# Performance work log

Hardware: AMD Instinct MI355X
Metric: run time of the kernel (lower is better)

## Reference

```python
import jax, jax.numpy as jnp
import numpy as np


def exp_mix_frac(p1, p2, a1, b1, a2, b2):
    # stable merge of two (numerator, denominator) pairs carried in log-scale p
    p = jnp.maximum(p1, p2)
    e1 = jnp.exp(p1 - p)
    e2 = jnp.exp(p2 - p)
    return a1 * e1 + a2 * e2, b1 * e1 + b2 * e2, p


def assoc_reduce_step(left, right):
    akv_l, ak_l, w_l, p_l = left
    akv_r, ak_r, w_r, p_r = right
    a, b, p = exp_mix_frac(p_l + w_r, p_r, akv_l, ak_l, akv_r, ak_r)
    return a, b, w_l + w_r, p


def setup_inputs() -> dict:
    key = jax.random.key(0)
    ks = jax.random.split(key, 7)
    S, B, E = 2048, 8, 1024
    scale = 1.0 / np.sqrt(E)
    return {
        "x": jax.random.normal(ks[0], (S, B, E), jnp.float32),
        "tmrkv": jax.random.uniform(ks[1], (3 * E,), jnp.float32),
        "Wk": jax.random.normal(ks[2], (E, E), jnp.float32) * scale,
        "Wv": jax.random.normal(ks[3], (E, E), jnp.float32) * scale,
        "time_decay": jax.random.normal(ks[4], (E,), jnp.float32) - 1.0,
        "time_first": jax.random.normal(ks[5], (E,), jnp.float32),
        "Wout": jax.random.normal(ks[6], (E, E), jnp.float32) * scale,
    }


def reference(x, tmrkv, Wk, Wv, time_decay, time_first, Wout):
    # x: (S, B, E) time-major (batch_first=False path of the source module)
    S, B, E = x.shape
    x_prev = jnp.concatenate([jnp.zeros_like(x[:1]), x[:-1]], axis=0)
    # time_mix_rkv layout: [r | k | v]; r-branch is computed in the source but
    # never used in the associative-scan path, so it is omitted (same output).
    mk = tmrkv[E:2 * E]
    mv = tmrkv[2 * E:]
    k = (mk * x + (1.0 - mk) * x_prev) @ Wk  # (S, B, E)
    v = (mv * x + (1.0 - mv) * x_prev) @ Wv  # (S, B, E)

    k_ = k.reshape(S, B * E)
    v_ = v.reshape(S, B * E)
    W_ = jnp.broadcast_to(jnp.tile(time_decay, B)[None, :], (S, B * E))
    ones = jnp.ones_like(v_)
    # log-depth parallel scan over time with numerically-stable exp merge
    a_, b_, _, p_ = jax.lax.associative_scan(
        assoc_reduce_step, (v_, ones, W_, k_), axis=0)

    a_state = a_.reshape(S, B, E)
    b_state = b_.reshape(S, B, E)
    p_state = p_.reshape(S, B, E)
    c, d, _ = exp_mix_frac(p_state, k + time_first + time_decay,
                           a_state, b_state, v, jnp.ones_like(v))
    rwkv = c / d  # (S, B, E)
    return rwkv @ Wout
```

## Files before the change

### kernel.cpp

```cpp
#include <hip/hip_runtime.h>
#include <stdint.h>

#define S_LEN  2048
#define B_DIM  8
#define E_DIM  1024
#define BE     (B_DIM * E_DIM)
#define M_ROWS (S_LEN * B_DIM)
#define NCHUNK 64
#define CLEN   (S_LEN / NCHUNK)

typedef __attribute__((ext_vector_type(8))) short bf16x8;
typedef __attribute__((ext_vector_type(4))) float f32x4;

__device__ __forceinline__ unsigned short f2bf(float f) {
    unsigned int u = __float_as_uint(f);
    u += 0x7FFFu + ((u >> 16) & 1u);
    return (unsigned short)(u >> 16);
}

__global__ __launch_bounds__(256) void mix_kernel(
    const float* __restrict__ x, const float* __restrict__ tmrkv,
    unsigned short* __restrict__ xk, unsigned short* __restrict__ xv)
{
    int i = blockIdx.x * 256 + threadIdx.x;
    const float4* x4 = (const float4*)x;
    float4 xc = x4[i];
    float4 xp = make_float4(0.f, 0.f, 0.f, 0.f);
    if (i >= BE / 4) xp = x4[i - BE / 4];
    int e4 = i & (E_DIM / 4 - 1);
    float4 mk = ((const float4*)(tmrkv + E_DIM))[e4];
    float4 mv = ((const float4*)(tmrkv + 2 * E_DIM))[e4];
    ushort4 ok, ov;
    ok.x = f2bf(mk.x * xc.x + (1.f - mk.x) * xp.x);
    ok.y = f2bf(mk.y * xc.y + (1.f - mk.y) * xp.y);
    ok.z = f2bf(mk.z * xc.z + (1.f - mk.z) * xp.z);
    ok.w = f2bf(mk.w * xc.w + (1.f - mk.w) * xp.w);
    ov.x = f2bf(mv.x * xc.x + (1.f - mv.x) * xp.x);
    ov.y = f2bf(mv.y * xc.y + (1.f - mv.y) * xp.y);
    ov.z = f2bf(mv.z * xc.z + (1.f - mv.z) * xp.z);
    ov.w = f2bf(mv.w * xc.w + (1.f - mv.w) * xp.w);
    ((ushort4*)xk)[i] = ok;
    ((ushort4*)xv)[i] = ov;
}

__global__ __launch_bounds__(256) void cast_transpose_k(
    const float* __restrict__ in, unsigned short* __restrict__ out)
{
    __shared__ float tile[32][33];
    int bx = blockIdx.x * 32, by = blockIdx.y * 32;
    int tx = threadIdx.x, ty = threadIdx.y;
    #pragma unroll
    for (int i = 0; i < 32; i += 8)
        tile[ty + i][tx] = in[(size_t)(by + ty + i) * E_DIM + bx + tx];
    __syncthreads();
    #pragma unroll
    for (int i = 0; i < 32; i += 8)
        out[(size_t)(bx + ty + i) * E_DIM + by + tx] = f2bf(tile[tx][ty + i]);
}

#define BM 128
#define BN 128
#define BK 32

__global__ __launch_bounds__(256) void gemm_bf16_bt(
    const unsigned short* __restrict__ A,
    const unsigned short* __restrict__ BT,
    float* __restrict__ C, int M, int N, int K)
{
    __shared__ __align__(16) unsigned short As[BM * BK];
    __shared__ __align__(16) unsigned short Bs[BN * BK];
    const int tid  = threadIdx.x;
    const int wave = tid >> 6, lane = tid & 63;
    const int bm = blockIdx.x * BM, bn = blockIdx.y * BN;
    const int wr = (wave >> 1) * 64, wc = (wave & 1) * 64;
    const int lrow = lane & 15, lq = lane >> 4;

    f32x4 acc[4][4];
    #pragma unroll
    for (int i = 0; i < 4; ++i)
        #pragma unroll
        for (int j = 0; j < 4; ++j)
            acc[i][j] = (f32x4){0.f, 0.f, 0.f, 0.f};

    const int nk = K / BK;
    for (int kt = 0; kt < nk; ++kt) {
        __syncthreads();
        const int kk = kt * BK;
        #pragma unroll
        for (int s = 0; s < 2; ++s) {
            int chunk = s * 256 + wave * 64 + lane;
            int row = chunk >> 2;
            int cb  = (chunk & 3) * 16;
            const char* ga = (const char*)(A  + (size_t)(bm + row) * K + kk) + cb;
            const char* gb = (const char*)(BT + (size_t)(bn + row) * K + kk) + cb;
            char* la = (char*)As + s * 4096 + wave * 1024;
            char* lb = (char*)Bs + s * 4096 + wave * 1024;
            __builtin_amdgcn_global_load_lds(
                (const __attribute__((address_space(1))) unsigned int*)ga,
                (__attribute__((address_space(3))) unsigned int*)la, 16, 0, 0);
            __builtin_amdgcn_global_load_lds(
                (const __attribute__((address_space(1))) unsigned int*)gb,
                (__attribute__((address_space(3))) unsigned int*)lb, 16, 0, 0);
        }
        __syncthreads();

        bf16x8 af[4], bf[4];
        #pragma unroll
        for (int i = 0; i < 4; ++i)
            af[i] = *(const bf16x8*)&As[(wr + i * 16 + lrow) * BK + lq * 8];
        #pragma unroll
        for (int j = 0; j < 4; ++j)
            bf[j] = *(const bf16x8*)&Bs[(wc + j * 16 + lrow) * BK + lq * 8];
        #pragma unroll
        for (int i = 0; i < 4; ++i)
            #pragma unroll
            for (int j = 0; j < 4; ++j)
                acc[i][j] = __builtin_amdgcn_mfma_f32_16x16x32_bf16(
                    af[i], bf[j], acc[i][j], 0, 0, 0);
    }

    #pragma unroll
    for (int i = 0; i < 4; ++i)
        #pragma unroll
        for (int j = 0; j < 4; ++j)
            #pragma unroll
            for (int r = 0; r < 4; ++r) {
                int row = bm + wr + i * 16 + lq * 4 + r;
                int col = bn + wc + j * 16 + lrow;
                C[(size_t)row * N + col] = acc[i][j][r];
            }
}

__global__ __launch_bounds__(256) void scan_pass1(
    const float* __restrict__ k, const float* __restrict__ v,
    const float* __restrict__ tdec,
    float* __restrict__ sA, float* __restrict__ sB, float* __restrict__ sP)
{
    int g  = blockIdx.x * 256 + threadIdx.x;
    int ch = g & (BE - 1);
    int c  = g >> 13;
    float w = tdec[ch & (E_DIM - 1)];
    size_t idx = (size_t)c * CLEN * BE + ch;
    float a = v[idx], bsum = 1.0f, p = k[idx];
    for (int j = 1; j < CLEN; ++j) {
        idx += BE;
        float kt = k[idx], vt = v[idx];
        float pw = p + w;
        float pn = fmaxf(pw, kt);
        float e1 = __expf(pw - pn), e2 = __expf(kt - pn);
        a    = a * e1 + vt * e2;
        bsum = bsum * e1 + e2;
        p    = pn;
    }
    sA[g] = a; sB[g] = bsum; sP[g] = p;
}

__global__ __launch_bounds__(256) void scan_pass2(
    const float* __restrict__ tdec,
    float* __restrict__ sA, float* __restrict__ sB, float* __restrict__ sP)
{
    int ch = blockIdx.x * 256 + threadIdx.x;
    float w  = tdec[ch & (E_DIM - 1)];
    float Lw = (float)CLEN * w;
    float pa = 0.f, pb = 0.f, pp = -__builtin_inff();
    for (int c = 0; c < NCHUNK; ++c) {
        int idx = c * BE + ch;
        float ra = sA[idx], rb = sB[idx], rp = sP[idx];
        sA[idx] = pa; sB[idx] = pb; sP[idx] = pp;
        float pw = pp + Lw;
        float pn = fmaxf(pw, rp);
        float e1 = __expf(pw - pn), e2 = __expf(rp - pn);
        pa = pa * e1 + ra * e2;
        pb = pb * e1 + rb * e2;
        pp = pn;
    }
}

__global__ __launch_bounds__(256) void scan_pass3(
    const float* __restrict__ k, const float* __restrict__ v,
    const float* __restrict__ tdec, const float* __restrict__ tfir,
    const float* __restrict__ sA, const float* __restrict__ sB,
    const float* __restrict__ sP, unsigned short* __restrict__ rwkv)
{
    int g  = blockIdx.x * 256 + threadIdx.x;
    int ch = g & (BE - 1);
    int c  = g >> 13;
    int e  = ch & (E_DIM - 1);
    float w  = tdec[e];
    float u2 = tfir[e] + w;
    float a = sA[g], bsum = sB[g], p = sP[g];
    size_t idx = (size_t)c * CLEN * BE + ch;
    for (int j = 0; j < CLEN; ++j) {
        float kt = k[idx], vt = v[idx];
        float pw = p + w;
        float pn = fmaxf(pw, kt);
        float e1 = __expf(pw - pn), e2 = __expf(kt - pn);
        a    = a * e1 + vt * e2;
        bsum = bsum * e1 + e2;
        p    = pn;
        float kb = kt + u2;
        float q  = fmaxf(p, kb);
        float f1 = __expf(p - q), f2 = __expf(kb - q);
        rwkv[idx] = f2bf((a * f1 + vt * f2) / (bsum * f1 + f2));
        idx += BE;
    }
}

extern "C" void kernel_launch(void* const* d_in, const int* in_sizes, int n_in,
                              void* d_out, int out_size, void* d_ws, size_t ws_size,
                              hipStream_t stream)
{
    const float* x     = (const float*)d_in[0];
    const float* tmrkv = (const float*)d_in[1];
    const float* Wk    = (const float*)d_in[2];
    const float* Wv    = (const float*)d_in[3];
    const float* tdec  = (const float*)d_in[4];
    const float* tfir  = (const float*)d_in[5];
    const float* Wout  = (const float*)d_in[6];
    float* out = (float*)d_out;

    char* ws = (char*)d_ws;
    const size_t SZ_XKV = (size_t)M_ROWS * E_DIM * 2;
    const size_t SZ_KV  = (size_t)M_ROWS * E_DIM * 4;
    unsigned short* xk   = (unsigned short*)(ws);
    unsigned short* xv   = (unsigned short*)(ws + SZ_XKV);
    float* kbuf          = (float*)(ws + 2 * SZ_XKV);
    float* vbuf          = (float*)(ws + 2 * SZ_XKV + SZ_KV);
    unsigned short* WkT  = (unsigned short*)(ws + 2 * SZ_XKV + 2 * SZ_KV);
    unsigned short* WvT  = WkT + (size_t)E_DIM * E_DIM;
    unsigned short* WoutT= WvT + (size_t)E_DIM * E_DIM;
    float* sA = (float*)xv;
    float* sB = sA + (size_t)NCHUNK * BE;
    float* sP = sB + (size_t)NCHUNK * BE;
    unsigned short* rwkv = xk;

    mix_kernel<<<(M_ROWS * E_DIM / 4) / 256, 256, 0, stream>>>(x, tmrkv, xk, xv);

    dim3 tb(32, 8), tg(E_DIM / 32, E_DIM / 32);
    cast_transpose_k<<<tg, tb, 0, stream>>>(Wk,   WkT);
    cast_transpose_k<<<tg, tb, 0, stream>>>(Wv,   WvT);
    cast_transpose_k<<<tg, tb, 0, stream>>>(Wout, WoutT);

    dim3 gg(M_ROWS / BM, E_DIM / BN);
    gemm_bf16_bt<<<gg, 256, 0, stream>>>(xk, WkT, kbuf, M_ROWS, E_DIM, E_DIM);
    gemm_bf16_bt<<<gg, 256, 0, stream>>>(xv, WvT, vbuf, M_ROWS, E_DIM, E_DIM);

    scan_pass1<<<(NCHUNK * BE) / 256, 256, 0, stream>>>(kbuf, vbuf, tdec, sA, sB, sP);
    scan_pass2<<<BE / 256, 256, 0, stream>>>(tdec, sA, sB, sP);
    scan_pass3<<<(NCHUNK * BE) / 256, 256, 0, stream>>>(kbuf, vbuf, tdec, tfir,
                                                        sA, sB, sP, rwkv);

    gemm_bf16_bt<<<gg, 256, 0, stream>>>(rwkv, WoutT, out, M_ROWS, E_DIM, E_DIM);
}
```

Measured before the change: 378.8 us.

## Double GEMM K-tile with XOR-swizzled LDS, parallelize chunk scan, batch weight transposes

Raises the GEMM K-tile from 32 to 64 and XOR-swizzles the 16-byte LDS chunks, so there are half as many barrier-separated iterations and fewer bank conflicts on the fragment reads. The serial 64-step carry scan in scan_pass2 becomes a wave-level log-depth shuffle scan over transposed data in shared memory, launched with four times as many blocks. The three weight cast-transposes are merged into one launch using blockIdx.z. The risks are a larger LDS footprint in the GEMM and more exp work in the parallel scan.

```diff
diff --git a/kernel.cpp b/kernel.cpp
--- a/kernel.cpp
+++ b/kernel.cpp
@@ -44,8 +44,13 @@
 }
 
 __global__ __launch_bounds__(256) void cast_transpose_k(
-    const float* __restrict__ in, unsigned short* __restrict__ out)
-{
+    const float* __restrict__ w0, const float* __restrict__ w1,
+    const float* __restrict__ w2,
+    unsigned short* __restrict__ o0, unsigned short* __restrict__ o1,
+    unsigned short* __restrict__ o2)
+{
+    const float* in = blockIdx.z == 0 ? w0 : (blockIdx.z == 1 ? w1 : w2);
+    unsigned short* out = blockIdx.z == 0 ? o0 : (blockIdx.z == 1 ? o1 : o2);
     __shared__ float tile[32][33];
     int bx = blockIdx.x * 32, by = blockIdx.y * 32;
     int tx = threadIdx.x, ty = threadIdx.y;
@@ -60,7 +65,7 @@
 
 #define BM 128
 #define BN 128
-#define BK 32
+#define BK 64
 
 __global__ __launch_bounds__(256) void gemm_bf16_bt(
     const unsigned short* __restrict__ A,
@@ -87,12 +92,12 @@
         __syncthreads();
         const int kk = kt * BK;
         #pragma unroll
-        for (int s = 0; s < 2; ++s) {
-            int chunk = s * 256 + wave * 64 + lane;
-            int row = chunk >> 2;
-            int cb  = (chunk & 3) * 16;
-            const char* ga = (const char*)(A  + (size_t)(bm + row) * K + kk) + cb;
-            const char* gb = (const char*)(BT + (size_t)(bn + row) * K + kk) + cb;
+        for (int s = 0; s < 4; ++s) {
+            int idx = s * 256 + wave * 64 + lane;
+            int r   = idx >> 3;
+            int gc  = (idx & 7) ^ (r & 7);
+            const char* ga = (const char*)(A  + (size_t)(bm + r) * K + kk) + gc * 16;
+            const char* gb = (const char*)(BT + (size_t)(bn + r) * K + kk) + gc * 16;
             char* la = (char*)As + s * 4096 + wave * 1024;
             char* lb = (char*)Bs + s * 4096 + wave * 1024;
             __builtin_amdgcn_global_load_lds(
@@ -104,19 +109,26 @@
         }
         __syncthreads();
 
-        bf16x8 af[4], bf[4];
-        #pragma unroll
-        for (int i = 0; i < 4; ++i)
-            af[i] = *(const bf16x8*)&As[(wr + i * 16 + lrow) * BK + lq * 8];
-        #pragma unroll
-        for (int j = 0; j < 4; ++j)
-            bf[j] = *(const bf16x8*)&Bs[(wc + j * 16 + lrow) * BK + lq * 8];
-        #pragma unroll
-        for (int i = 0; i < 4; ++i)
+        #pragma unroll
+        for (int h = 0; h < 2; ++h) {
+            bf16x8 af[4], bf[4];
             #pragma unroll
-            for (int j = 0; j < 4; ++j)
-                acc[i][j] = __builtin_amdgcn_mfma_f32_16x16x32_bf16(
-                    af[i], bf[j], acc[i][j], 0, 0, 0);
+            for (int i = 0; i < 4; ++i) {
+                int R = wr + i * 16 + lrow;
+                af[i] = *(const bf16x8*)&As[R * BK + (((h << 2) | lq) ^ (R & 7)) * 8];
+            }
+            #pragma unroll
+            for (int j = 0; j < 4; ++j) {
+                int R = wc + j * 16 + lrow;
+                bf[j] = *(const bf16x8*)&Bs[R * BK + (((h << 2) | lq) ^ (R & 7)) * 8];
+            }
+            #pragma unroll
+            for (int i = 0; i < 4; ++i)
+                #pragma unroll
+                for (int j = 0; j < 4; ++j)
+                    acc[i][j] = __builtin_amdgcn_mfma_f32_16x16x32_bf16(
+                        af[i], bf[j], acc[i][j], 0, 0, 0);
+        }
     }
 
     #pragma unroll
@@ -159,20 +171,60 @@
     const float* __restrict__ tdec,
     float* __restrict__ sA, float* __restrict__ sB, float* __restrict__ sP)
 {
-    int ch = blockIdx.x * 256 + threadIdx.x;
-    float w  = tdec[ch & (E_DIM - 1)];
-    float Lw = (float)CLEN * w;
-    float pa = 0.f, pb = 0.f, pp = -__builtin_inff();
-    for (int c = 0; c < NCHUNK; ++c) {
-        int idx = c * BE + ch;
-        float ra = sA[idx], rb = sB[idx], rp = sP[idx];
-        sA[idx] = pa; sB[idx] = pb; sP[idx] = pp;
-        float pw = pp + Lw;
-        float pn = fmaxf(pw, rp);
-        float e1 = __expf(pw - pn), e2 = __expf(rp - pn);
-        pa = pa * e1 + ra * e2;
-        pb = pb * e1 + rb * e2;
-        pp = pn;
+    __shared__ float tA[64 * 65], tB[64 * 65], tP[64 * 65];
+    const int t   = threadIdx.x;
+    const int ch0 = blockIdx.x * 64;
+    const int chl = t & 63;
+    const int cq  = t >> 6;
+    #pragma unroll 4
+    for (int cc = 0; cc < 16; ++cc) {
+        int c = cq * 16 + cc;
+        int idx = c * BE + ch0 + chl;
+        tA[chl * 65 + c] = sA[idx];
+        tB[chl * 65 + c] = sB[idx];
+        tP[chl * 65 + c] = sP[idx];
+    }
+    __syncthreads();
+    const int lane = t & 63, wave = t >> 6;
+    for (int i = 0; i < 16; ++i) {
+        int ch = wave * 16 + i;
+        float w = tdec[(ch0 + ch) & (E_DIM - 1)];
+        float a = tA[ch * 65 + lane];
+        float b = tB[ch * 65 + lane];
+        float p = tP[ch * 65 + lane];
+        float W = (float)CLEN * w;
+        #pragma unroll
+        for (int d = 1; d < 64; d <<= 1) {
+            float a_l = __shfl_up(a, d);
+            float b_l = __shfl_up(b, d);
+            float p_l = __shfl_up(p, d);
+            float W_l = __shfl_up(W, d);
+            if (lane >= d) {
+                float pw = p_l + W;
+                float pn = fmaxf(pw, p);
+                float e1 = __expf(pw - pn), e2 = __expf(p - pn);
+                a = a_l * e1 + a * e2;
+                b = b_l * e1 + b * e2;
+                p = pn;
+                W = W_l + W;
+            }
+        }
+        float ea = __shfl_up(a, 1);
+        float eb = __shfl_up(b, 1);
+        float ep = __shfl_up(p, 1);
+        if (lane == 0) { ea = 0.f; eb = 0.f; ep = -__builtin_inff(); }
+        tA[ch * 65 + lane] = ea;
+        tB[ch * 65 + lane] = eb;
+        tP[ch * 65 + lane] = ep;
+    }
+    __syncthreads();
+    #pragma unroll 4
+    for (int cc = 0; cc < 16; ++cc) {
+        int c = cq * 16 + cc;
+        int idx = c * BE + ch0 + chl;
+        sA[idx] = tA[chl * 65 + c];
+        sB[idx] = tB[chl * 65 + c];
+        sP[idx] = tP[chl * 65 + c];
     }
 }
 
@@ -236,17 +288,15 @@
 
     mix_kernel<<<(M_ROWS * E_DIM / 4) / 256, 256, 0, stream>>>(x, tmrkv, xk, xv);
 
-    dim3 tb(32, 8), tg(E_DIM / 32, E_DIM / 32);
-    cast_transpose_k<<<tg, tb, 0, stream>>>(Wk,   WkT);
-    cast_transpose_k<<<tg, tb, 0, stream>>>(Wv,   WvT);
-    cast_transpose_k<<<tg, tb, 0, stream>>>(Wout, WoutT);
+    dim3 tb(32, 8), tg(E_DIM / 32, E_DIM / 32, 3);
+    cast_transpose_k<<<tg, tb, 0, stream>>>(Wk, Wv, Wout, WkT, WvT, WoutT);
 
     dim3 gg(M_ROWS / BM, E_DIM / BN);
     gemm_bf16_bt<<<gg, 256, 0, stream>>>(xk, WkT, kbuf, M_ROWS, E_DIM, E_DIM);
     gemm_bf16_bt<<<gg, 256, 0, stream>>>(xv, WvT, vbuf, M_ROWS, E_DIM, E_DIM);
 
     scan_pass1<<<(NCHUNK * BE) / 256, 256, 0, stream>>>(kbuf, vbuf, tdec, sA, sB, sP);
-    scan_pass2<<<BE / 256, 256, 0, stream>>>(tdec, sA, sB, sP);
+    scan_pass2<<<BE / 64, 256, 0, stream>>>(tdec, sA, sB, sP);
     scan_pass3<<<(NCHUNK * BE) / 256, 256, 0, stream>>>(kbuf, vbuf, tdec, tfir,
                                                         sA, sB, sP, rwkv);
 
```

After: 346.3 us. 1.09x faster.
